# Kernel optimization log

Hardware: AMD Instinct MI355X
Metric: run time of the kernel (lower is better)

## Reference

```python
import jax, jax.numpy as jnp
import numpy as np

ROLL, N, F_IN, H, F_OUT = 200, 4096, 5, 32, 1


def setup_inputs() -> dict:
    key = jax.random.key(0)
    ks = jax.random.split(key, 12)
    s = 0.1
    return {
        "X": jax.random.normal(ks[0], (ROLL, N, F_IN), dtype=jnp.float32),
        "A": jax.random.uniform(ks[1], (N, N), dtype=jnp.float32) / N,  # row-normalized-ish adjacency
        "Wx": jax.random.normal(ks[2], (F_IN, H), dtype=jnp.float32) * s,
        "Wh": jax.random.normal(ks[3], (H, H), dtype=jnp.float32) * s,
        "Wc": jax.random.normal(ks[4], (H, H), dtype=jnp.float32) * s,
        "W_ih": jax.random.normal(ks[5], (4 * H, H), dtype=jnp.float32) * s,
        "W_hh": jax.random.normal(ks[6], (4 * H, H), dtype=jnp.float32) * s,
        "b_ih": jax.random.normal(ks[7], (4 * H,), dtype=jnp.float32) * s,
        "b_hh": jax.random.normal(ks[8], (4 * H,), dtype=jnp.float32) * s,
        "W_fc": jax.random.normal(ks[9], (F_OUT, H), dtype=jnp.float32) * s,
        "b_fc": jax.random.normal(ks[10], (F_OUT,), dtype=jnp.float32) * s,
    }


def reference(X, A, Wx, Wh, Wc, W_ih, W_hh, b_ih, b_hh, W_fc, b_fc):
    N_, H_ = A.shape[0], Wh.shape[0]

    def step(carry, xt):
        h, c = carry
        # GCN layers: (A @ X) @ W, matching torch's left-to-right A @ X @ W
        x_gcn = (A @ xt) @ Wx        # [N, H]
        h_gcn = (A @ h) @ Wh         # [N, H]
        c_gcn = (A @ c) @ Wc         # [N, H]
        inp = x_gcn + h_gcn + c_gcn  # LSTMCell input
        # torch.nn.LSTMCell: gates = inp @ W_ih.T + b_ih + h @ W_hh.T + b_hh
        gates = inp @ W_ih.T + b_ih + h @ W_hh.T + b_hh  # [N, 4H]
        i, f, g, o = jnp.split(gates, 4, axis=-1)
        i = jax.nn.sigmoid(i)
        f = jax.nn.sigmoid(f)
        g = jnp.tanh(g)
        o = jax.nn.sigmoid(o)
        c_new = f * c + i * g
        h_new = o * jnp.tanh(c_new)
        return (h_new, c_new), None

    h0 = jnp.zeros((N_, H_), dtype=X.dtype)
    c0 = jnp.zeros((N_, H_), dtype=X.dtype)
    (h_final, _), _ = jax.lax.scan(step, (h0, c0), X)
    return h_final @ W_fc.T + b_fc  # [N, 1]
```

## Files before the change

kernel.cpp:

```cpp
#include <hip/hip_runtime.h>

#define N_NODES 4096
#define H_DIM 32
#define F_INPUT 5
#define ROLLS 200
#define NBLK 256
#define NBUF 64
#define MT_ELEMS ((size_t)H_DIM * N_NODES)

typedef __attribute__((ext_vector_type(8))) short bf16x8;
typedef __attribute__((ext_vector_type(4))) float fx4;

__device__ __forceinline__ unsigned short f2bf(float f) {
  unsigned int u = __builtin_bit_cast(unsigned int, f);
  u += 0x7fffu + ((u >> 16) & 1u);
  return (unsigned short)(u >> 16);
}

__device__ __forceinline__ void wait_all(const unsigned* flags, int tid,
                                         unsigned target) {
  if (tid < 64) {
    for (;;) {
      bool ok = true;
#pragma unroll
      for (int j = 0; j < 4; ++j) {
        unsigned v = __hip_atomic_load(&flags[tid * 4 + j], __ATOMIC_RELAXED,
                                       __HIP_MEMORY_SCOPE_AGENT);
        ok = ok && (v >= target);
      }
      if (__ballot(ok) == ~0ull) break;
      __builtin_amdgcn_s_sleep(1);
    }
  }
  __syncthreads();
  asm volatile("" ::: "memory");
}

__device__ __forceinline__ void store_mt_block(unsigned short* mtblk,
                                               const unsigned short* tile,
                                               int lane) {
  int h = lane >> 1, half = lane & 1;
  unsigned* dst = (unsigned*)mtblk + lane * 4;
#pragma unroll
  for (int j = 0; j < 4; ++j) {
    unsigned lo = tile[(half * 8 + 2 * j) * 48 + h];
    unsigned hi = tile[(half * 8 + 2 * j + 1) * 48 + h];
    __hip_atomic_store(dst + j, lo | (hi << 16), __ATOMIC_RELAXED,
                       __HIP_MEMORY_SCOPE_AGENT);
  }
}

__global__ __launch_bounds__(512, 2) void k_roll(
    const float* __restrict__ A, const float* __restrict__ X,
    const float* __restrict__ Wx, const float* __restrict__ Wh, const float* __restrict__ Wc,
    const float* __restrict__ Wih, const float* __restrict__ Whh,
    const float* __restrict__ b_ih, const float* __restrict__ b_hh,
    const float* __restrict__ Wfc, const float* __restrict__ b_fc,
    float* __restrict__ out,
    unsigned short* __restrict__ bufs, unsigned* __restrict__ flags) {

  __shared__ __align__(16) float red[8 * 16 * 33];
  __shared__ __align__(16) unsigned short inpB[16 * 48];
  __shared__ __align__(16) unsigned short hB[16 * 48];
  __shared__ __align__(16) unsigned short cnB[16 * 48];
  __shared__ __align__(16) unsigned short MnB[16 * 48];
  __shared__ __align__(16) float cB[16 * 32];
  __shared__ __align__(16) float gatesLds[16 * 132];
  __shared__ __align__(16) float xLds[16 * 8];

  const int tid  = threadIdx.x;
  const int wave = tid >> 6;
  const int lane = tid & 63;
  const int l15  = lane & 15;
  const int quad = lane >> 4;
  const int bid  = blockIdx.x;
  const int row0 = bid << 4;

  bf16x8 areg[16];
  {
    const float* Ap = A + (size_t)(row0 + l15) * N_NODES + wave * 512 + quad * 8;
#pragma unroll
    for (int kk = 0; kk < 16; ++kk) {
      bf16x8 a;
#pragma unroll
      for (int j = 0; j < 8; ++j) a[j] = (short)f2bf(Ap[kk * 32 + j]);
      areg[kk] = a;
    }
  }

  const int g = (wave << 4) + l15;
  bf16x8 bI, bH;
#pragma unroll
  for (int j = 0; j < 8; ++j) {
    bI[j] = (short)f2bf(Wih[g * 32 + quad * 8 + j]);
    bH[j] = (short)f2bf(Whh[g * 32 + quad * 8 + j]);
  }
  const float bias = b_ih[g] + b_hh[g];

  bf16x8 bWh, bWc;
  float wx5[F_INPUT];
  if (wave < 2) {
#pragma unroll
    for (int j = 0; j < 8; ++j) {
      bWh[j] = (short)f2bf(Wh[(quad * 8 + j) * H_DIM + g]);
      bWc[j] = (short)f2bf(Wc[(quad * 8 + j) * H_DIM + g]);
    }
#pragma unroll
    for (int f = 0; f < F_INPUT; ++f) wx5[f] = Wx[f * H_DIM + g];
  }

  {
    int r = tid >> 5, k = tid & 31;
    hB[r * 48 + k] = 0;
    cB[r * 32 + k] = 0.f;
    float s = 0.f;
#pragma unroll
    for (int f = 0; f < F_INPUT; ++f)
      s += X[(size_t)(row0 + r) * F_INPUT + f] * Wx[f * H_DIM + k];
    MnB[r * 48 + k] = f2bf(s);
  }
  __syncthreads();
  if (wave == 0) {
    store_mt_block(bufs + (size_t)bid * 512, MnB, lane);
    asm volatile("s_waitcnt vmcnt(0)" ::: "memory");
    if (lane == 0)
      __hip_atomic_store(&flags[bid], 1u, __ATOMIC_RELAXED,
                         __HIP_MEMORY_SCOPE_AGENT);
  }

  for (int t = 0; t < ROLLS; ++t) {
    const unsigned short* m0 = bufs + (size_t)(t & (NBUF - 1)) * MT_ELEMS;
    unsigned short* m1 = bufs + (size_t)((t + 1) & (NBUF - 1)) * MT_ELEMS;

    if ((t & (NBUF - 1)) == 0) {
      __syncthreads();
      if (tid < 64)
        __builtin_amdgcn_fence(__ATOMIC_ACQUIRE, "agent");
      __syncthreads();
    }

    wait_all(flags, tid, (unsigned)(t + 1));

    if (t + 1 < ROLLS && tid < 128) {
      int r = tid >> 3, f = tid & 7;
      if (f < F_INPUT)
        xLds[r * 8 + f] = X[(size_t)(t + 1) * N_NODES * F_INPUT +
                            (size_t)(row0 + r) * F_INPUT + f];
    }

    fx4 acc0 = {0.f, 0.f, 0.f, 0.f}, acc1 = {0.f, 0.f, 0.f, 0.f};
    {
      const unsigned short* Bb = m0 + ((wave << 5) + (quad >> 1)) * 512
                                    + l15 * 16 + (quad & 1) * 8;
      bf16x8 b0s[16], b1s[16];
#pragma unroll
      for (int s = 0; s < 16; ++s) {
        b0s[s] = *(const bf16x8*)(Bb + s * 1024);
        b1s[s] = *(const bf16x8*)(Bb + s * 1024 + 256);
      }
      __builtin_amdgcn_sched_barrier(0);
#pragma unroll
      for (int s = 0; s < 16; ++s) {
        acc0 = __builtin_amdgcn_mfma_f32_16x16x32_bf16(areg[s], b0s[s], acc0, 0, 0, 0);
        acc1 = __builtin_amdgcn_mfma_f32_16x16x32_bf16(areg[s], b1s[s], acc1, 0, 0, 0);
      }
    }
#pragma unroll
    for (int r = 0; r < 4; ++r) {
      red[(wave * 16 + quad * 4 + r) * 33 + l15]      = acc0[r];
      red[(wave * 16 + quad * 4 + r) * 33 + 16 + l15] = acc1[r];
    }
    __syncthreads();

    {
      int m = tid >> 5, n = tid & 31;
      float s = 0.f;
#pragma unroll
      for (int w = 0; w < 8; ++w) s += red[(w * 16 + m) * 33 + n];
      inpB[m * 48 + n] = f2bf(s);
    }
    __syncthreads();

    {
      bf16x8 aI = *(const bf16x8*)(inpB + l15 * 48 + quad * 8);
      bf16x8 aH = *(const bf16x8*)(hB   + l15 * 48 + quad * 8);
      fx4 gacc = {0.f, 0.f, 0.f, 0.f};
      gacc = __builtin_amdgcn_mfma_f32_16x16x32_bf16(aI, bI, gacc, 0, 0, 0);
      gacc = __builtin_amdgcn_mfma_f32_16x16x32_bf16(aH, bH, gacc, 0, 0, 0);
#pragma unroll
      for (int r = 0; r < 4; ++r) gatesLds[(quad * 4 + r) * 132 + g] = gacc[r] + bias;
    }
    __syncthreads();

    {
      int r = tid >> 5, k = tid & 31;
      float gi = gatesLds[r * 132 + k];
      float gf = gatesLds[r * 132 + 32 + k];
      float gg = gatesLds[r * 132 + 64 + k];
      float go = gatesLds[r * 132 + 96 + k];
      float i_ = 1.f / (1.f + __expf(-gi));
      float f_ = 1.f / (1.f + __expf(-gf));
      float g_ = tanhf(gg);
      float o_ = 1.f / (1.f + __expf(-go));
      float cn = f_ * cB[r * 32 + k] + i_ * g_;
      float hn = o_ * tanhf(cn);
      cB[r * 32 + k] = cn;
      hB[r * 48 + k] = f2bf(hn);
      cnB[r * 48 + k] = f2bf(cn);
      if (t == ROLLS - 1) gatesLds[r * 132 + k] = hn * Wfc[k];
    }
    __syncthreads();

    if (t < ROLLS - 1) {
      if (wave < 2) {
        bf16x8 aH = *(const bf16x8*)(hB  + l15 * 48 + quad * 8);
        bf16x8 aC = *(const bf16x8*)(cnB + l15 * 48 + quad * 8);
        fx4 m4 = {0.f, 0.f, 0.f, 0.f};
        m4 = __builtin_amdgcn_mfma_f32_16x16x32_bf16(aH, bWh, m4, 0, 0, 0);
        m4 = __builtin_amdgcn_mfma_f32_16x16x32_bf16(aC, bWc, m4, 0, 0, 0);
#pragma unroll
        for (int r = 0; r < 4; ++r) {
          int m = quad * 4 + r;
          float xs = m4[r];
#pragma unroll
          for (int f = 0; f < F_INPUT; ++f) xs += xLds[m * 8 + f] * wx5[f];
          MnB[m * 48 + g] = f2bf(xs);
        }
      }
      __syncthreads();
      if (wave == 0) {
        store_mt_block(m1 + (size_t)bid * 512, MnB, lane);
        asm volatile("s_waitcnt vmcnt(0)" ::: "memory");
        if (lane == 0)
          __hip_atomic_store(&flags[bid], (unsigned)(t + 2), __ATOMIC_RELAXED,
                             __HIP_MEMORY_SCOPE_AGENT);
      }
    }
  }

  if (tid < 16) {
    float s = b_fc[0];
#pragma unroll
    for (int k = 0; k < 32; ++k) s += gatesLds[tid * 132 + k];
    out[row0 + tid] = s;
  }
}

extern "C" void kernel_launch(void* const* d_in, const int* in_sizes, int n_in,
                              void* d_out, int out_size, void* d_ws, size_t ws_size,
                              hipStream_t stream) {
  (void)in_sizes; (void)n_in; (void)out_size; (void)ws_size;
  const float* X   = (const float*)d_in[0];
  const float* A   = (const float*)d_in[1];
  const float* Wx  = (const float*)d_in[2];
  const float* Wh  = (const float*)d_in[3];
  const float* Wc  = (const float*)d_in[4];
  const float* Wih = (const float*)d_in[5];
  const float* Whh = (const float*)d_in[6];
  const float* bih = (const float*)d_in[7];
  const float* bhh = (const float*)d_in[8];
  const float* Wfc = (const float*)d_in[9];
  const float* bfc = (const float*)d_in[10];
  float* outp = (float*)d_out;

  char* ws = (char*)d_ws;
  unsigned short* bufs = (unsigned short*)ws;
  ws += (size_t)NBUF * MT_ELEMS * 2;
  unsigned* flags = (unsigned*)ws;
  ws += NBLK * sizeof(unsigned);

  (void)hipMemsetAsync(flags, 0, NBLK * sizeof(unsigned), stream);

  void* args[] = {
    (void*)&A, (void*)&X, (void*)&Wx, (void*)&Wh, (void*)&Wc,
    (void*)&Wih, (void*)&Whh, (void*)&bih, (void*)&bhh,
    (void*)&Wfc, (void*)&bfc, (void*)&outp,
    (void*)&bufs, (void*)&flags
  };
  (void)hipLaunchCooperativeKernel((const void*)k_roll, dim3(NBLK), dim3(512),
                                   args, 0, stream);
}
```

Baseline: 1.751 ms.

## Shrink per-step critical path with per-wave flag waits and two-wave LDS barriers

Each wave now polls only the 32 flags of the producer blocks whose slice it reads, so it can start its MFMA work without waiting for every block and without a block-wide barrier. The gate GEMM, LSTM activations and next-step message computation are folded into two waves synchronised by LDS atomic counters instead of several __syncthreads, removing three full-block barriers per step. The reduction padding and store layout are also changed to reduce LDS bank conflicts and improve store coalescing. The risk lies in spin-wait correctness and ordering across waves, for example LDS reuse between iterations when the other six waves run ahead.

```diff
diff --git a/kernel.cpp b/kernel.cpp
--- a/kernel.cpp
+++ b/kernel.cpp
@@ -17,35 +17,43 @@
   return (unsigned short)(u >> 16);
 }
 
-__device__ __forceinline__ void wait_all(const unsigned* flags, int tid,
-                                         unsigned target) {
-  if (tid < 64) {
-    for (;;) {
-      bool ok = true;
-#pragma unroll
-      for (int j = 0; j < 4; ++j) {
-        unsigned v = __hip_atomic_load(&flags[tid * 4 + j], __ATOMIC_RELAXED,
-                                       __HIP_MEMORY_SCOPE_AGENT);
-        ok = ok && (v >= target);
-      }
-      if (__ballot(ok) == ~0ull) break;
-      __builtin_amdgcn_s_sleep(1);
-    }
-  }
-  __syncthreads();
+__device__ __forceinline__ void wait_group(const unsigned* flags, int wave,
+                                           int lane, unsigned target) {
+  const unsigned* f = flags + (wave << 5) + (lane & 31);
+  for (;;) {
+    unsigned v = __hip_atomic_load(f, __ATOMIC_RELAXED,
+                                   __HIP_MEMORY_SCOPE_AGENT);
+    if (__ballot(v >= target) == ~0ull) break;
+    __builtin_amdgcn_s_sleep(1);
+  }
   asm volatile("" ::: "memory");
+  __builtin_amdgcn_sched_barrier(0);
+}
+
+__device__ __forceinline__ void pair_bar(unsigned* ctr, int lane,
+                                         unsigned want) {
+  asm volatile("s_waitcnt lgkmcnt(0)" ::: "memory");
+  if (lane == 0)
+    __hip_atomic_fetch_add(ctr, 1u, __ATOMIC_RELAXED,
+                           __HIP_MEMORY_SCOPE_WORKGROUP);
+  while (__hip_atomic_load(ctr, __ATOMIC_RELAXED,
+                           __HIP_MEMORY_SCOPE_WORKGROUP) < want) {}
+  asm volatile("" ::: "memory");
+  __builtin_amdgcn_sched_barrier(0);
 }
 
 __device__ __forceinline__ void store_mt_block(unsigned short* mtblk,
                                                const unsigned short* tile,
                                                int lane) {
-  int h = lane >> 1, half = lane & 1;
-  unsigned* dst = (unsigned*)mtblk + lane * 4;
+  unsigned* base = (unsigned*)mtblk;
 #pragma unroll
   for (int j = 0; j < 4; ++j) {
-    unsigned lo = tile[(half * 8 + 2 * j) * 48 + h];
-    unsigned hi = tile[(half * 8 + 2 * j + 1) * 48 + h];
-    __hip_atomic_store(dst + j, lo | (hi << 16), __ATOMIC_RELAXED,
+    int d = j * 64 + lane;
+    int h = d >> 3;
+    int rr = 2 * (d & 7);
+    unsigned lo = tile[rr * 48 + h];
+    unsigned hi = tile[(rr + 1) * 48 + h];
+    __hip_atomic_store(base + d, lo | (hi << 16), __ATOMIC_RELAXED,
                        __HIP_MEMORY_SCOPE_AGENT);
   }
 }
@@ -59,14 +67,13 @@
     float* __restrict__ out,
     unsigned short* __restrict__ bufs, unsigned* __restrict__ flags) {
 
-  __shared__ __align__(16) float red[8 * 16 * 33];
-  __shared__ __align__(16) unsigned short inpB[16 * 48];
-  __shared__ __align__(16) unsigned short hB[16 * 48];
+  __shared__ __align__(16) float red[8 * 16 * 36];
+  __shared__ __align__(16) unsigned short hnB[16 * 48];
   __shared__ __align__(16) unsigned short cnB[16 * 48];
   __shared__ __align__(16) unsigned short MnB[16 * 48];
-  __shared__ __align__(16) float cB[16 * 32];
-  __shared__ __align__(16) float gatesLds[16 * 132];
   __shared__ __align__(16) float xLds[16 * 8];
+  __shared__ __align__(16) float hFin[16 * 32];
+  __shared__ unsigned pb[3];
 
   const int tid  = threadIdx.x;
   const int wave = tid >> 6;
@@ -88,31 +95,34 @@
     }
   }
 
-  const int g = (wave << 4) + l15;
-  bf16x8 bI, bH;
-#pragma unroll
-  for (int j = 0; j < 8; ++j) {
-    bI[j] = (short)f2bf(Wih[g * 32 + quad * 8 + j]);
-    bH[j] = (short)f2bf(Whh[g * 32 + quad * 8 + j]);
-  }
-  const float bias = b_ih[g] + b_hh[g];
-
-  bf16x8 bWh, bWc;
-  float wx5[F_INPUT];
+  const int kcol = (wave << 4) + l15;
+  bf16x8 bIq[4], bHq[4], bWh, bWc;
+  float biasq[4], wx5[F_INPUT];
   if (wave < 2) {
 #pragma unroll
+    for (int q = 0; q < 4; ++q) {
+      int n = q * 32 + kcol;
+#pragma unroll
+      for (int j = 0; j < 8; ++j) {
+        bIq[q][j] = (short)f2bf(Wih[n * 32 + quad * 8 + j]);
+        bHq[q][j] = (short)f2bf(Whh[n * 32 + quad * 8 + j]);
+      }
+      biasq[q] = b_ih[n] + b_hh[n];
+    }
+#pragma unroll
     for (int j = 0; j < 8; ++j) {
-      bWh[j] = (short)f2bf(Wh[(quad * 8 + j) * H_DIM + g]);
-      bWc[j] = (short)f2bf(Wc[(quad * 8 + j) * H_DIM + g]);
-    }
-#pragma unroll
-    for (int f = 0; f < F_INPUT; ++f) wx5[f] = Wx[f * H_DIM + g];
-  }
-
+      bWh[j] = (short)f2bf(Wh[(quad * 8 + j) * H_DIM + kcol]);
+      bWc[j] = (short)f2bf(Wc[(quad * 8 + j) * H_DIM + kcol]);
+    }
+#pragma unroll
+    for (int f = 0; f < F_INPUT; ++f) wx5[f] = Wx[f * H_DIM + kcol];
+  }
+  fx4 c4 = {0.f, 0.f, 0.f, 0.f};
+
+  for (int i = tid; i < 16 * 48; i += 512) hnB[i] = 0;
+  if (tid == 0) { pb[0] = 0; pb[1] = 0; pb[2] = 0; }
   {
     int r = tid >> 5, k = tid & 31;
-    hB[r * 48 + k] = 0;
-    cB[r * 32 + k] = 0.f;
     float s = 0.f;
 #pragma unroll
     for (int f = 0; f < F_INPUT; ++f)
@@ -139,7 +149,7 @@
       __syncthreads();
     }
 
-    wait_all(flags, tid, (unsigned)(t + 1));
+    wait_group(flags, wave, lane, (unsigned)(t + 1));
 
     if (t + 1 < ROLLS && tid < 128) {
       int r = tid >> 3, f = tid & 7;
@@ -167,82 +177,86 @@
     }
 #pragma unroll
     for (int r = 0; r < 4; ++r) {
-      red[(wave * 16 + quad * 4 + r) * 33 + l15]      = acc0[r];
-      red[(wave * 16 + quad * 4 + r) * 33 + 16 + l15] = acc1[r];
+      red[(wave * 16 + quad * 4 + r) * 36 + l15]      = acc0[r];
+      red[(wave * 16 + quad * 4 + r) * 36 + 16 + l15] = acc1[r];
     }
     __syncthreads();
 
-    {
-      int m = tid >> 5, n = tid & 31;
-      float s = 0.f;
-#pragma unroll
-      for (int w = 0; w < 8; ++w) s += red[(w * 16 + m) * 33 + n];
-      inpB[m * 48 + n] = f2bf(s);
-    }
-    __syncthreads();
-
-    {
-      bf16x8 aI = *(const bf16x8*)(inpB + l15 * 48 + quad * 8);
-      bf16x8 aH = *(const bf16x8*)(hB   + l15 * 48 + quad * 8);
-      fx4 gacc = {0.f, 0.f, 0.f, 0.f};
-      gacc = __builtin_amdgcn_mfma_f32_16x16x32_bf16(aI, bI, gacc, 0, 0, 0);
-      gacc = __builtin_amdgcn_mfma_f32_16x16x32_bf16(aH, bH, gacc, 0, 0, 0);
-#pragma unroll
-      for (int r = 0; r < 4; ++r) gatesLds[(quad * 4 + r) * 132 + g] = gacc[r] + bias;
-    }
-    __syncthreads();
-
-    {
-      int r = tid >> 5, k = tid & 31;
-      float gi = gatesLds[r * 132 + k];
-      float gf = gatesLds[r * 132 + 32 + k];
-      float gg = gatesLds[r * 132 + 64 + k];
-      float go = gatesLds[r * 132 + 96 + k];
-      float i_ = 1.f / (1.f + __expf(-gi));
-      float f_ = 1.f / (1.f + __expf(-gf));
-      float g_ = tanhf(gg);
-      float o_ = 1.f / (1.f + __expf(-go));
-      float cn = f_ * cB[r * 32 + k] + i_ * g_;
-      float hn = o_ * tanhf(cn);
-      cB[r * 32 + k] = cn;
-      hB[r * 48 + k] = f2bf(hn);
-      cnB[r * 48 + k] = f2bf(cn);
-      if (t == ROLLS - 1) gatesLds[r * 132 + k] = hn * Wfc[k];
-    }
-    __syncthreads();
-
-    if (t < ROLLS - 1) {
-      if (wave < 2) {
-        bf16x8 aH = *(const bf16x8*)(hB  + l15 * 48 + quad * 8);
-        bf16x8 aC = *(const bf16x8*)(cnB + l15 * 48 + quad * 8);
+    if (wave < 2) {
+      const unsigned want = 2u * (unsigned)(t + 1);
+      bf16x8 aI;
+#pragma unroll
+      for (int j = 0; j < 8; ++j) {
+        int n = quad * 8 + j;
+        float s = 0.f;
+#pragma unroll
+        for (int w = 0; w < 8; ++w) s += red[(w * 16 + l15) * 36 + n];
+        aI[j] = (short)f2bf(s);
+      }
+      bf16x8 aH = *(const bf16x8*)(hnB + l15 * 48 + quad * 8);
+      pair_bar(&pb[0], lane, want);
+
+      fx4 gq0 = {0,0,0,0}, gq1 = {0,0,0,0}, gq2 = {0,0,0,0}, gq3 = {0,0,0,0};
+      gq0 = __builtin_amdgcn_mfma_f32_16x16x32_bf16(aI, bIq[0], gq0, 0, 0, 0);
+      gq0 = __builtin_amdgcn_mfma_f32_16x16x32_bf16(aH, bHq[0], gq0, 0, 0, 0);
+      gq1 = __builtin_amdgcn_mfma_f32_16x16x32_bf16(aI, bIq[1], gq1, 0, 0, 0);
+      gq1 = __builtin_amdgcn_mfma_f32_16x16x32_bf16(aH, bHq[1], gq1, 0, 0, 0);
+      gq2 = __builtin_amdgcn_mfma_f32_16x16x32_bf16(aI, bIq[2], gq2, 0, 0, 0);
+      gq2 = __builtin_amdgcn_mfma_f32_16x16x32_bf16(aH, bHq[2], gq2, 0, 0, 0);
+      gq3 = __builtin_amdgcn_mfma_f32_16x16x32_bf16(aI, bIq[3], gq3, 0, 0, 0);
+      gq3 = __builtin_amdgcn_mfma_f32_16x16x32_bf16(aH, bHq[3], gq3, 0, 0, 0);
+
+#pragma unroll
+      for (int r = 0; r < 4; ++r) {
+        int m = quad * 4 + r;
+        float gi = gq0[r] + biasq[0];
+        float gf = gq1[r] + biasq[1];
+        float gg = gq2[r] + biasq[2];
+        float go = gq3[r] + biasq[3];
+        float i_ = 1.f / (1.f + __expf(-gi));
+        float f_ = 1.f / (1.f + __expf(-gf));
+        float g_ = tanhf(gg);
+        float o_ = 1.f / (1.f + __expf(-go));
+        float cn = f_ * c4[r] + i_ * g_;
+        float hn = o_ * tanhf(cn);
+        c4[r] = cn;
+        hnB[m * 48 + kcol] = f2bf(hn);
+        cnB[m * 48 + kcol] = f2bf(cn);
+        if (t == ROLLS - 1) hFin[m * 32 + kcol] = hn;
+      }
+      pair_bar(&pb[1], lane, want);
+
+      if (t < ROLLS - 1) {
+        bf16x8 aHn = *(const bf16x8*)(hnB + l15 * 48 + quad * 8);
+        bf16x8 aCn = *(const bf16x8*)(cnB + l15 * 48 + quad * 8);
         fx4 m4 = {0.f, 0.f, 0.f, 0.f};
-        m4 = __builtin_amdgcn_mfma_f32_16x16x32_bf16(aH, bWh, m4, 0, 0, 0);
-        m4 = __builtin_amdgcn_mfma_f32_16x16x32_bf16(aC, bWc, m4, 0, 0, 0);
+        m4 = __builtin_amdgcn_mfma_f32_16x16x32_bf16(aHn, bWh, m4, 0, 0, 0);
+        m4 = __builtin_amdgcn_mfma_f32_16x16x32_bf16(aCn, bWc, m4, 0, 0, 0);
 #pragma unroll
         for (int r = 0; r < 4; ++r) {
           int m = quad * 4 + r;
           float xs = m4[r];
 #pragma unroll
           for (int f = 0; f < F_INPUT; ++f) xs += xLds[m * 8 + f] * wx5[f];
-          MnB[m * 48 + g] = f2bf(xs);
+          MnB[m * 48 + kcol] = f2bf(xs);
         }
-      }
-      __syncthreads();
-      if (wave == 0) {
-        store_mt_block(m1 + (size_t)bid * 512, MnB, lane);
-        asm volatile("s_waitcnt vmcnt(0)" ::: "memory");
-        if (lane == 0)
-          __hip_atomic_store(&flags[bid], (unsigned)(t + 2), __ATOMIC_RELAXED,
-                             __HIP_MEMORY_SCOPE_AGENT);
-      }
-    }
-  }
-
-  if (tid < 16) {
+        pair_bar(&pb[2], lane, want);
+        if (wave == 0) {
+          store_mt_block(m1 + (size_t)bid * 512, MnB, lane);
+          asm volatile("s_waitcnt vmcnt(0)" ::: "memory");
+          if (lane == 0)
+            __hip_atomic_store(&flags[bid], (unsigned)(t + 2), __ATOMIC_RELAXED,
+                               __HIP_MEMORY_SCOPE_AGENT);
+        }
+      }
+    }
+  }
+
+  if (wave == 0 && lane < 16) {
     float s = b_fc[0];
 #pragma unroll
-    for (int k = 0; k < 32; ++k) s += gatesLds[tid * 132 + k];
-    out[row0 + tid] = s;
+    for (int k = 0; k < 32; ++k) s += hFin[lane * 32 + k] * Wfc[k];
+    out[row0 + lane] = s;
   }
 }
 
```

New measurement: 2.145 ms. 1.23x slower.

## Cut per-step barriers: direct global stores from MFMA waves, fused reduction, register cell state

Applied to the files above, without the earlier changes.

The two MFMA waves now write their bf16 output fragments straight to the global exchange buffer and each bump the block flag with an atomic add. This removes the LDS staging tile, one barrier and the single-wave store, and the wait target doubles to match. The cross-wave reduction now reads vectorised fx4 rows from a padded LDS array and builds the MFMA A operand directly in registers, which drops the inpB buffer and another barrier. Cell state is held in a register instead of LDS, at the cost of two flag atomics per block per step.

```diff
diff --git a/kernel.cpp b/kernel.cpp
--- a/kernel.cpp
+++ b/kernel.cpp
@@ -34,20 +34,6 @@
   }
   __syncthreads();
   asm volatile("" ::: "memory");
-}
-
-__device__ __forceinline__ void store_mt_block(unsigned short* mtblk,
-                                               const unsigned short* tile,
-                                               int lane) {
-  int h = lane >> 1, half = lane & 1;
-  unsigned* dst = (unsigned*)mtblk + lane * 4;
-#pragma unroll
-  for (int j = 0; j < 4; ++j) {
-    unsigned lo = tile[(half * 8 + 2 * j) * 48 + h];
-    unsigned hi = tile[(half * 8 + 2 * j + 1) * 48 + h];
-    __hip_atomic_store(dst + j, lo | (hi << 16), __ATOMIC_RELAXED,
-                       __HIP_MEMORY_SCOPE_AGENT);
-  }
 }
 
 __global__ __launch_bounds__(512, 2) void k_roll(
@@ -59,12 +45,9 @@
     float* __restrict__ out,
     unsigned short* __restrict__ bufs, unsigned* __restrict__ flags) {
 
-  __shared__ __align__(16) float red[8 * 16 * 33];
-  __shared__ __align__(16) unsigned short inpB[16 * 48];
+  __shared__ __align__(16) float red[8 * 16 * 36];
   __shared__ __align__(16) unsigned short hB[16 * 48];
   __shared__ __align__(16) unsigned short cnB[16 * 48];
-  __shared__ __align__(16) unsigned short MnB[16 * 48];
-  __shared__ __align__(16) float cB[16 * 32];
   __shared__ __align__(16) float gatesLds[16 * 132];
   __shared__ __align__(16) float xLds[16 * 8];
 
@@ -109,23 +92,32 @@
     for (int f = 0; f < F_INPUT; ++f) wx5[f] = Wx[f * H_DIM + g];
   }
 
+  float c_reg = 0.f;
+
+  for (int i = tid; i < 16 * 48; i += 512) hB[i] = 0;
   {
     int r = tid >> 5, k = tid & 31;
-    hB[r * 48 + k] = 0;
-    cB[r * 32 + k] = 0.f;
     float s = 0.f;
 #pragma unroll
     for (int f = 0; f < F_INPUT; ++f)
       s += X[(size_t)(row0 + r) * F_INPUT + f] * Wx[f * H_DIM + k];
-    MnB[r * 48 + k] = f2bf(s);
+    gatesLds[r * 132 + k] = s;
   }
   __syncthreads();
-  if (wave == 0) {
-    store_mt_block(bufs + (size_t)bid * 512, MnB, lane);
+  if (wave < 2) {
+    unsigned short us[4];
+#pragma unroll
+    for (int r = 0; r < 4; ++r)
+      us[r] = f2bf(gatesLds[(quad * 4 + r) * 132 + g]);
+    unsigned long long v = (unsigned long long)(us[0] | ((unsigned)us[1] << 16))
+                         | ((unsigned long long)(us[2] | ((unsigned)us[3] << 16)) << 32);
+    char* slot = (char*)(bufs + (size_t)bid * 512);
+    __hip_atomic_store((unsigned long long*)(slot + g * 32 + quad * 8), v,
+                       __ATOMIC_RELAXED, __HIP_MEMORY_SCOPE_AGENT);
     asm volatile("s_waitcnt vmcnt(0)" ::: "memory");
     if (lane == 0)
-      __hip_atomic_store(&flags[bid], 1u, __ATOMIC_RELAXED,
-                         __HIP_MEMORY_SCOPE_AGENT);
+      __hip_atomic_fetch_add(&flags[bid], 1u, __ATOMIC_RELAXED,
+                             __HIP_MEMORY_SCOPE_AGENT);
   }
 
   for (int t = 0; t < ROLLS; ++t) {
@@ -139,7 +131,7 @@
       __syncthreads();
     }
 
-    wait_all(flags, tid, (unsigned)(t + 1));
+    wait_all(flags, tid, 2u * (unsigned)(t + 1));
 
     if (t + 1 < ROLLS && tid < 128) {
       int r = tid >> 3, f = tid & 7;
@@ -167,23 +159,26 @@
     }
 #pragma unroll
     for (int r = 0; r < 4; ++r) {
-      red[(wave * 16 + quad * 4 + r) * 33 + l15]      = acc0[r];
-      red[(wave * 16 + quad * 4 + r) * 33 + 16 + l15] = acc1[r];
+      red[(wave * 16 + quad * 4 + r) * 36 + l15]      = acc0[r];
+      red[(wave * 16 + quad * 4 + r) * 36 + 16 + l15] = acc1[r];
     }
     __syncthreads();
 
     {
-      int m = tid >> 5, n = tid & 31;
-      float s = 0.f;
-#pragma unroll
-      for (int w = 0; w < 8; ++w) s += red[(w * 16 + m) * 33 + n];
-      inpB[m * 48 + n] = f2bf(s);
-    }
-    __syncthreads();
-
-    {
-      bf16x8 aI = *(const bf16x8*)(inpB + l15 * 48 + quad * 8);
-      bf16x8 aH = *(const bf16x8*)(hB   + l15 * 48 + quad * 8);
+      fx4 sum0 = {0.f, 0.f, 0.f, 0.f}, sum1 = {0.f, 0.f, 0.f, 0.f};
+#pragma unroll
+      for (int w = 0; w < 8; ++w) {
+        const fx4* p = (const fx4*)&red[((w << 4) + l15) * 36 + quad * 8];
+        sum0 += p[0];
+        sum1 += p[1];
+      }
+      bf16x8 aI;
+#pragma unroll
+      for (int j = 0; j < 4; ++j) {
+        aI[j]     = (short)f2bf(sum0[j]);
+        aI[4 + j] = (short)f2bf(sum1[j]);
+      }
+      bf16x8 aH = *(const bf16x8*)(hB + l15 * 48 + quad * 8);
       fx4 gacc = {0.f, 0.f, 0.f, 0.f};
       gacc = __builtin_amdgcn_mfma_f32_16x16x32_bf16(aI, bI, gacc, 0, 0, 0);
       gacc = __builtin_amdgcn_mfma_f32_16x16x32_bf16(aH, bH, gacc, 0, 0, 0);
@@ -202,42 +197,43 @@
       float f_ = 1.f / (1.f + __expf(-gf));
       float g_ = tanhf(gg);
       float o_ = 1.f / (1.f + __expf(-go));
-      float cn = f_ * cB[r * 32 + k] + i_ * g_;
+      float cn = f_ * c_reg + i_ * g_;
       float hn = o_ * tanhf(cn);
-      cB[r * 32 + k] = cn;
-      hB[r * 48 + k] = f2bf(hn);
+      c_reg = cn;
+      hB[r * 48 + k]  = f2bf(hn);
       cnB[r * 48 + k] = f2bf(cn);
       if (t == ROLLS - 1) gatesLds[r * 132 + k] = hn * Wfc[k];
     }
     __syncthreads();
 
-    if (t < ROLLS - 1) {
-      if (wave < 2) {
-        bf16x8 aH = *(const bf16x8*)(hB  + l15 * 48 + quad * 8);
-        bf16x8 aC = *(const bf16x8*)(cnB + l15 * 48 + quad * 8);
-        fx4 m4 = {0.f, 0.f, 0.f, 0.f};
-        m4 = __builtin_amdgcn_mfma_f32_16x16x32_bf16(aH, bWh, m4, 0, 0, 0);
-        m4 = __builtin_amdgcn_mfma_f32_16x16x32_bf16(aC, bWc, m4, 0, 0, 0);
-#pragma unroll
-        for (int r = 0; r < 4; ++r) {
-          int m = quad * 4 + r;
-          float xs = m4[r];
-#pragma unroll
-          for (int f = 0; f < F_INPUT; ++f) xs += xLds[m * 8 + f] * wx5[f];
-          MnB[m * 48 + g] = f2bf(xs);
-        }
-      }
-      __syncthreads();
-      if (wave == 0) {
-        store_mt_block(m1 + (size_t)bid * 512, MnB, lane);
-        asm volatile("s_waitcnt vmcnt(0)" ::: "memory");
-        if (lane == 0)
-          __hip_atomic_store(&flags[bid], (unsigned)(t + 2), __ATOMIC_RELAXED,
-                             __HIP_MEMORY_SCOPE_AGENT);
-      }
-    }
-  }
-
+    if (t < ROLLS - 1 && wave < 2) {
+      bf16x8 aHn = *(const bf16x8*)(hB  + l15 * 48 + quad * 8);
+      bf16x8 aCn = *(const bf16x8*)(cnB + l15 * 48 + quad * 8);
+      fx4 m4 = {0.f, 0.f, 0.f, 0.f};
+      m4 = __builtin_amdgcn_mfma_f32_16x16x32_bf16(aHn, bWh, m4, 0, 0, 0);
+      m4 = __builtin_amdgcn_mfma_f32_16x16x32_bf16(aCn, bWc, m4, 0, 0, 0);
+      unsigned short us[4];
+#pragma unroll
+      for (int r = 0; r < 4; ++r) {
+        float xs = m4[r];
+#pragma unroll
+        for (int f = 0; f < F_INPUT; ++f)
+          xs += xLds[(quad * 4 + r) * 8 + f] * wx5[f];
+        us[r] = f2bf(xs);
+      }
+      unsigned long long v = (unsigned long long)(us[0] | ((unsigned)us[1] << 16))
+                           | ((unsigned long long)(us[2] | ((unsigned)us[3] << 16)) << 32);
+      char* slot = (char*)(m1 + (size_t)bid * 512);
+      __hip_atomic_store((unsigned long long*)(slot + g * 32 + quad * 8), v,
+                         __ATOMIC_RELAXED, __HIP_MEMORY_SCOPE_AGENT);
+      asm volatile("s_waitcnt vmcnt(0)" ::: "memory");
+      if (lane == 0)
+        __hip_atomic_fetch_add(&flags[bid], 1u, __ATOMIC_RELAXED,
+                               __HIP_MEMORY_SCOPE_AGENT);
+    }
+  }
+
+  __syncthreads();
   if (tid < 16) {
     float s = b_fc[0];
 #pragma unroll
```

After: 2.102 ms. 1.2x slower.
